# Optimization experiments

Hardware: AMD Instinct MI355X
Metric: run time of the kernel (lower is better)

## Reference

```python
import jax, jax.numpy as jnp
import numpy as np
import math

B, T, D = 4, 8192, 512
E, K, F = 8, 2, 2048
CAP_FACTOR = 1.25


def setup_inputs() -> dict:
    key = jax.random.key(0)
    ks = jax.random.split(key, 4)
    return {
        "x": jax.random.normal(ks[0], (B, T, D), jnp.float32),
        "gate_w": jax.random.normal(ks[1], (E, D), jnp.float32) * 0.01,  # std=0.01 init
        "w1": jax.random.normal(ks[2], (E, D, F), jnp.float32) * (1.0 / np.sqrt(D)),
        "b1": jnp.zeros((E, F), jnp.float32),
        "w2": jax.random.normal(ks[3], (E, F, D), jnp.float32) * (1.0 / np.sqrt(F)),
        "b2": jnp.zeros((E, D), jnp.float32),
    }


def reference(x, gate_w, w1, b1, w2, b2):
    Bx, Tx, Dx = x.shape
    N = Bx * Tx
    C = math.ceil(CAP_FACTOR * N / E)  # per-expert capacity
    xf = x.reshape(N, Dx)

    # --- Router (eval mode: no noise) ---
    probs = jax.nn.softmax(xf @ gate_w.T, axis=-1)            # (N, E)
    topk_vals, topk_idx = jax.lax.top_k(probs, K)             # (N, K)
    topk_vals = topk_vals / topk_vals.sum(-1, keepdims=True)

    # --- Capacity-based dispatch: token-major, k-minor assignment order,
    #     matching the original serial double loop exactly. ---
    flat_e = topk_idx.reshape(N * K)                          # (NK,)
    onehot = jax.nn.one_hot(flat_e, E, dtype=jnp.int32)       # (NK, E)
    # slot within expert = number of earlier assignments to same expert
    pos = jnp.cumsum(onehot, axis=0)[jnp.arange(N * K), flat_e] - 1
    keep = pos < C                                            # tokens over capacity are dropped
    pos_safe = jnp.where(keep, pos, C)                        # route drops to pad slot C
    token_ids = jnp.repeat(jnp.arange(N), K)

    # --- Gather tokens into (E, C, D) expert buffers (slot C is trash) ---
    buf = jnp.zeros((E, C + 1, Dx), x.dtype).at[flat_e, pos_safe].set(xf[token_ids])
    expert_in = buf[:, :C]                                    # (E, C, D)

    # --- Per-expert FFN (exact GELU, dropout=0 in eval) ---
    h = jax.nn.gelu(jnp.einsum('ecd,edf->ecf', expert_in, w1) + b1[:, None, :],
                    approximate=False)                        # (E, C, F)
    expert_out = jnp.einsum('ecf,efd->ecd', h, w2) + b2[:, None, :]  # (E, C, D)

    # --- Weighted combine back to tokens ---
    gathered = expert_out[flat_e, jnp.minimum(pos_safe, C - 1)]      # (NK, D)
    w = (topk_vals.reshape(N * K) * keep).astype(x.dtype)            # zero for dropped
    out = (gathered * w[:, None]).reshape(N, K, Dx).sum(axis=1)      # (N, D)
    return out.reshape(Bx, Tx, Dx)
```

## Files before the change

kernel.cpp:

```cpp
#include <hip/hip_runtime.h>
#include <math.h>

#define Bx 4
#define Tt 8192
#define Nn (Bx * Tt)
#define Dd 512
#define Ee 8
#define Kk 2
#define Ff 2048
#define Cc 5120
#define NK (Nn * Kk)

typedef unsigned short ushort_t;
typedef __attribute__((ext_vector_type(8))) short bf16x8;
typedef __attribute__((ext_vector_type(4))) float f32x4;

__device__ __forceinline__ float gelu_exact(float v) {
    return 0.5f * v * (1.0f + erff(v * 0.70710678118654752440f));
}

__device__ __forceinline__ ushort_t f2bf(float f) {
    union { float f; unsigned u; } v; v.f = f;
    unsigned r = v.u + 0x7fffu + ((v.u >> 16) & 1u);
    return (ushort_t)(r >> 16);
}

__device__ __forceinline__ void gload_lds16(const ushort_t* g, short* l) {
    __builtin_amdgcn_global_load_lds(
        (const __attribute__((address_space(1))) unsigned int*)g,
        (__attribute__((address_space(3))) unsigned int*)l, 16, 0, 0);
}

__global__ __launch_bounds__(256) void moe_gate_kernel(
    const float* __restrict__ x, const float* __restrict__ gate_w,
    int* __restrict__ flat_e, float* __restrict__ wArr) {
    __shared__ float gw[Ee * Dd];
    int tid = threadIdx.x;
    for (int i = tid; i < 1024; i += 256)
        ((float4*)gw)[i] = ((const float4*)gate_w)[i];
    __syncthreads();

    int wave = tid >> 6, lane = tid & 63;
    int token = blockIdx.x * 4 + wave;

    const float4* xr = (const float4*)(x + (size_t)token * Dd);
    float4 xa = xr[lane];
    float4 xb = xr[lane + 64];

    float acc[Ee];
#pragma unroll
    for (int e = 0; e < Ee; e++) {
        const float4* g = (const float4*)(gw + e * Dd);
        float4 ga = g[lane], gb = g[lane + 64];
        acc[e] = xa.x * ga.x + xa.y * ga.y + xa.z * ga.z + xa.w * ga.w +
                 xb.x * gb.x + xb.y * gb.y + xb.z * gb.z + xb.w * gb.w;
    }
#pragma unroll
    for (int off = 32; off >= 1; off >>= 1) {
#pragma unroll
        for (int e = 0; e < Ee; e++) acc[e] += __shfl_xor(acc[e], off, 64);
    }

    if (lane == 0) {
        float m = acc[0];
#pragma unroll
        for (int e = 1; e < Ee; e++) m = fmaxf(m, acc[e]);
        float p[Ee], s = 0.f;
#pragma unroll
        for (int e = 0; e < Ee; e++) { p[e] = expf(acc[e] - m); s += p[e]; }
        int i0 = 0;
#pragma unroll
        for (int e = 1; e < Ee; e++) if (p[e] > p[i0]) i0 = e;
        int i1 = (i0 == 0) ? 1 : 0;
#pragma unroll
        for (int e = 0; e < Ee; e++) if (e != i0 && p[e] > p[i1]) i1 = e;
        float v0 = p[i0] / s, v1 = p[i1] / s;
        float inv = 1.f / (v0 + v1);
        flat_e[token * 2 + 0] = i0;
        flat_e[token * 2 + 1] = i1;
        wArr[token * 2 + 0] = v0 * inv;
        wArr[token * 2 + 1] = v1 * inv;
    }
}

__global__ __launch_bounds__(256) void moe_hist_kernel(
    const int* __restrict__ flat_e, int* __restrict__ blockCounts) {
    __shared__ int cnt[Ee];
    int tid = threadIdx.x;
    if (tid < Ee) cnt[tid] = 0;
    __syncthreads();
    int e = flat_e[blockIdx.x * 256 + tid];
    atomicAdd(&cnt[e], 1);
    __syncthreads();
    if (tid < Ee) blockCounts[blockIdx.x * Ee + tid] = cnt[tid];
}

__global__ void moe_scan_kernel(const int* __restrict__ blockCounts,
                                int* __restrict__ blockOffsets,
                                int* __restrict__ counts) {
    int e = threadIdx.x;
    if (e >= Ee) return;
    int run = 0;
    for (int b = 0; b < 256; b++) {
        blockOffsets[b * Ee + e] = run;
        run += blockCounts[b * Ee + e];
    }
    counts[e] = min(run, Cc);
}

__global__ __launch_bounds__(256) void moe_scatter_kernel(
    const int* __restrict__ flat_e, const float* __restrict__ wArr,
    const int* __restrict__ blockOffsets,
    int* __restrict__ srcOf, float* __restrict__ wSlot) {
    __shared__ int waveCnt[4][Ee];
    int tid = threadIdx.x;
    int i = blockIdx.x * 256 + tid;
    int e = flat_e[i];
    int wv = tid >> 6, lane = tid & 63;
    unsigned long long ltmask = (1ull << lane) - 1ull;
    int myrank = 0;
#pragma unroll
    for (int ee = 0; ee < Ee; ee++) {
        unsigned long long m = __ballot(e == ee);
        if (e == ee) myrank = __popcll(m & ltmask);
        if (lane == 0) waveCnt[wv][ee] = __popcll(m);
    }
    __syncthreads();
    int base = blockOffsets[blockIdx.x * Ee + e];
    for (int w = 0; w < wv; w++) base += waveCnt[w][e];
    int pos = base + myrank;
    if (pos < Cc) {
        srcOf[e * Cc + pos] = i >> 1;
        wSlot[e * Cc + pos] = wArr[i];
    }
}

__global__ __launch_bounds__(256) void moe_transpose_kernel(
    const float* __restrict__ in, ushort_t* __restrict__ out, int R, int Cn) {
    __shared__ float t[32][33];
    int ez = blockIdx.z;
    const float* ine = in + (size_t)ez * R * Cn;
    ushort_t* oute = out + (size_t)ez * R * Cn;
    int tx = threadIdx.x & 31, ty = threadIdx.x >> 5;
    int r0 = blockIdx.y * 32, c0 = blockIdx.x * 32;
#pragma unroll
    for (int j = 0; j < 4; j++)
        t[ty + j * 8][tx] = ine[(size_t)(r0 + ty + j * 8) * Cn + c0 + tx];
    __syncthreads();
#pragma unroll
    for (int j = 0; j < 4; j++)
        oute[(size_t)(c0 + ty + j * 8) * R + r0 + tx] = f2bf(t[tx][ty + j * 8]);
}

__global__ __launch_bounds__(256) void moe_gather_kernel(
    const float* __restrict__ x, const int* __restrict__ srcOf,
    const int* __restrict__ counts, int chunk0, ushort_t* __restrict__ xg) {
    int tid = threadIdx.x, wave = tid >> 6, lane = tid & 63;
    int sl = blockIdx.x * 4 + wave;
    int le = sl / Cc, c = sl - le * Cc;
    int e = chunk0 + le;
    int cnt = counts[e];
    ushort_t* dst = xg + (size_t)sl * Dd + lane * 8;
    uint4 o;
    if (c < cnt) {
        int src = srcOf[e * Cc + c];
        const float4* xr = (const float4*)(x + (size_t)src * Dd + lane * 8);
        float4 v0 = xr[0], v1 = xr[1];
        o.x = (unsigned)f2bf(v0.x) | ((unsigned)f2bf(v0.y) << 16);
        o.y = (unsigned)f2bf(v0.z) | ((unsigned)f2bf(v0.w) << 16);
        o.z = (unsigned)f2bf(v1.x) | ((unsigned)f2bf(v1.y) << 16);
        o.w = (unsigned)f2bf(v1.z) | ((unsigned)f2bf(v1.w) << 16);
    } else {
        o = make_uint4(0, 0, 0, 0);
    }
    *(uint4*)dst = o;
}


__global__ __launch_bounds__(256) void moe_mfma_gemm1(
    const ushort_t* __restrict__ xg, const ushort_t* __restrict__ w1t,
    const float* __restrict__ b1, int chunk0, ushort_t* __restrict__ hbuf) {
    int le = blockIdx.z, e = chunk0 + le;
    const ushort_t* A = xg + (size_t)le * Cc * Dd;
    const ushort_t* Bt = w1t + (size_t)e * Ff * Dd;
    const float* bias = b1 + (size_t)e * Ff;
    ushort_t* h = hbuf + (size_t)le * Cc * Ff;

    __shared__ short Al[4 * 128 * 8];
    __shared__ short Bl[4 * 128 * 8];

    int tid = threadIdx.x;
    int lane = tid & 63, wave = tid >> 6;
    int wr = wave >> 1, wc = wave & 1;
    int m0 = blockIdx.y * 128;
    int n0 = blockIdx.x * 128;
    int kslot = lane >> 4, lr = lane & 15;
    int aoff = (kslot * 128 + wr * 64 + lr) * 8;
    int boff = (kslot * 128 + wc * 64 + lr) * 8;
    int wbase = (tid & 192) * 8;

    f32x4 acc[4][4] = {};

    for (int k0 = 0; k0 < Dd; k0 += 32) {
#pragma unroll
        for (int p = 0; p < 2; ++p) {
            int id = p * 256 + tid;
            int ks = id >> 7, row = id & 127;
            gload_lds16(A + (size_t)(m0 + row) * Dd + k0 + ks * 8,
                        &Al[p * 2048 + wbase]);
            gload_lds16(Bt + (size_t)(n0 + row) * Dd + k0 + ks * 8,
                        &Bl[p * 2048 + wbase]);
        }
        __syncthreads();
        bf16x8 a[4], b[4];
#pragma unroll
        for (int m = 0; m < 4; ++m) a[m] = *(const bf16x8*)&Al[aoff + m * 128];
#pragma unroll
        for (int n = 0; n < 4; ++n) b[n] = *(const bf16x8*)&Bl[boff + n * 128];
#pragma unroll
        for (int m = 0; m < 4; ++m)
#pragma unroll
            for (int n = 0; n < 4; ++n)
                acc[m][n] = __builtin_amdgcn_mfma_f32_16x16x32_bf16(
                    a[m], b[n], acc[m][n], 0, 0, 0);
        __syncthreads();
    }

    float bv[4];
#pragma unroll
    for (int n = 0; n < 4; ++n) bv[n] = bias[n0 + wc * 64 + n * 16 + lr];
#pragma unroll
    for (int m = 0; m < 4; ++m) {
#pragma unroll
        for (int r = 0; r < 4; ++r) {
            int row = m0 + wr * 64 + m * 16 + kslot * 4 + r;
            size_t base = (size_t)row * Ff + n0 + wc * 64 + lr;
#pragma unroll
            for (int n = 0; n < 4; ++n)
                h[base + n * 16] = f2bf(gelu_exact(acc[m][n][r] + bv[n]));
        }
    }
}

__global__ __launch_bounds__(256) void moe_mfma_gemm2(
    const ushort_t* __restrict__ hbuf, const ushort_t* __restrict__ w2t,
    const float* __restrict__ b2, const int* __restrict__ srcOf,
    const float* __restrict__ wSlot, const int* __restrict__ counts,
    int chunk0, float* __restrict__ out) {
    int le = blockIdx.z, e = chunk0 + le;
    const ushort_t* A = hbuf + (size_t)le * Cc * Ff;
    const ushort_t* Bt = w2t + (size_t)e * Dd * Ff;
    const float* bias = b2 + (size_t)e * Dd;
    const int* srcE = srcOf + (size_t)e * Cc;
    const float* wE = wSlot + (size_t)e * Cc;
    int count = counts[e];

    __shared__ short Al[4 * 128 * 8];
    __shared__ short Bl[4 * 128 * 8];

    int tid = threadIdx.x;
    int lane = tid & 63, wave = tid >> 6;
    int wr = wave >> 1, wc = wave & 1;
    int m0 = blockIdx.y * 128;
    int n0 = blockIdx.x * 128;
    int kslot = lane >> 4, lr = lane & 15;
    int aoff = (kslot * 128 + wr * 64 + lr) * 8;
    int boff = (kslot * 128 + wc * 64 + lr) * 8;
    int wbase = (tid & 192) * 8;

    f32x4 acc[4][4] = {};

    for (int k0 = 0; k0 < Ff; k0 += 32) {
#pragma unroll
        for (int p = 0; p < 2; ++p) {
            int id = p * 256 + tid;
            int ks = id >> 7, row = id & 127;
            gload_lds16(A + (size_t)(m0 + row) * Ff + k0 + ks * 8,
                        &Al[p * 2048 + wbase]);
            gload_lds16(Bt + (size_t)(n0 + row) * Ff + k0 + ks * 8,
                        &Bl[p * 2048 + wbase]);
        }
        __syncthreads();
        bf16x8 a[4], b[4];
#pragma unroll
        for (int m = 0; m < 4; ++m) a[m] = *(const bf16x8*)&Al[aoff + m * 128];
#pragma unroll
        for (int n = 0; n < 4; ++n) b[n] = *(const bf16x8*)&Bl[boff + n * 128];
#pragma unroll
        for (int m = 0; m < 4; ++m)
#pragma unroll
            for (int n = 0; n < 4; ++n)
                acc[m][n] = __builtin_amdgcn_mfma_f32_16x16x32_bf16(
                    a[m], b[n], acc[m][n], 0, 0, 0);
        __syncthreads();
    }

    float bv[4];
#pragma unroll
    for (int n = 0; n < 4; ++n) bv[n] = bias[n0 + wc * 64 + n * 16 + lr];
#pragma unroll
    for (int m = 0; m < 4; ++m) {
#pragma unroll
        for (int r = 0; r < 4; ++r) {
            int row = m0 + wr * 64 + m * 16 + kslot * 4 + r;
            if (row < count) {
                int token = srcE[row];
                float wgt = wE[row];
                float* op = out + (size_t)token * Dd + n0 + wc * 64 + lr;
#pragma unroll
                for (int n = 0; n < 4; ++n)
                    atomicAdd(&op[n * 16], wgt * (acc[m][n][r] + bv[n]));
            }
        }
    }
}

extern "C" void kernel_launch(void* const* d_in, const int* in_sizes, int n_in,
                              void* d_out, int out_size, void* d_ws, size_t ws_size,
                              hipStream_t stream) {
    const float* x      = (const float*)d_in[0];
    const float* gate_w = (const float*)d_in[1];
    const float* w1     = (const float*)d_in[2];
    const float* b1     = (const float*)d_in[3];
    const float* w2     = (const float*)d_in[4];
    const float* b2     = (const float*)d_in[5];
    float* out = (float*)d_out;

    char* p = (char*)d_ws;
    int*      flat_e       = (int*)p;       p += (size_t)NK * 4;
    float*    wArr         = (float*)p;     p += (size_t)NK * 4;
    int*      blockCounts  = (int*)p;       p += 256 * Ee * 4;
    int*      blockOffsets = (int*)p;       p += 256 * Ee * 4;
    int*      counts       = (int*)p;       p += 64 * 4;
    int*      srcOf        = (int*)p;       p += (size_t)Ee * Cc * 4;
    float*    wSlot        = (float*)p;     p += (size_t)Ee * Cc * 4;
    p = (char*)(((size_t)p + 255) & ~(size_t)255);
    ushort_t* w1t          = (ushort_t*)p;  p += (size_t)Ee * Dd * Ff * 2;
    ushort_t* w2t          = (ushort_t*)p;  p += (size_t)Ee * Ff * Dd * 2;
    size_t fixedEnd = (size_t)(p - (char*)d_ws);
    size_t avail = (ws_size > fixedEnd) ? ws_size - fixedEnd : 0;

    size_t perE = (size_t)Cc * Dd * 2 + (size_t)Cc * Ff * 2;
    int P = Ee;
    while (P > 1 && (size_t)P * perE > avail) P >>= 1;
    ushort_t* xg = (ushort_t*)((char*)d_ws + fixedEnd);
    ushort_t* hbuf = xg + (size_t)P * Cc * Dd;

    moe_gate_kernel<<<Nn / 4, 256, 0, stream>>>(x, gate_w, flat_e, wArr);
    moe_hist_kernel<<<NK / 256, 256, 0, stream>>>(flat_e, blockCounts);
    moe_scan_kernel<<<1, 64, 0, stream>>>(blockCounts, blockOffsets, counts);
    moe_scatter_kernel<<<NK / 256, 256, 0, stream>>>(flat_e, wArr, blockOffsets,
                                                     srcOf, wSlot);
    moe_transpose_kernel<<<dim3(Ff / 32, Dd / 32, Ee), 256, 0, stream>>>(
        w1, w1t, Dd, Ff);
    moe_transpose_kernel<<<dim3(Dd / 32, Ff / 32, Ee), 256, 0, stream>>>(
        w2, w2t, Ff, Dd);
    hipMemsetAsync(d_out, 0, (size_t)Nn * Dd * sizeof(float), stream);

    for (int c0 = 0; c0 < Ee; c0 += P) {
        moe_gather_kernel<<<P * Cc / 4, 256, 0, stream>>>(x, srcOf, counts, c0, xg);
        moe_mfma_gemm1<<<dim3(Ff / 128, Cc / 128, P), 256, 0, stream>>>(
            xg, w1t, b1, c0, hbuf);
        moe_mfma_gemm2<<<dim3(Dd / 128, Cc / 128, P), 256, 0, stream>>>(
            hbuf, w2t, b2, srcOf, wSlot, counts, c0, out);
    }
}
```

Baseline: 685.8 us.

## Double-buffer LDS staging in both GEMMs and split-K gemm2 across two blocks

```diff
diff --git a/kernel.cpp b/kernel.cpp
--- a/kernel.cpp
+++ b/kernel.cpp
@@ -177,6 +177,15 @@
 }
 
 
+#define GSTAGE(gA, gB, Al, Bl, buf, t, wbase)                                  \
+    do {                                                                       \
+        int _k = (t) * 32;                                                     \
+        gload_lds16((gA) + _k,      &(Al)[(buf) * 4096 + (wbase)]);            \
+        gload_lds16((gA) + _k + 16, &(Al)[(buf) * 4096 + 2048 + (wbase)]);     \
+        gload_lds16((gB) + _k,      &(Bl)[(buf) * 4096 + (wbase)]);            \
+        gload_lds16((gB) + _k + 16, &(Bl)[(buf) * 4096 + 2048 + (wbase)]);     \
+    } while (0)
+
 __global__ __launch_bounds__(256) void moe_mfma_gemm1(
     const ushort_t* __restrict__ xg, const ushort_t* __restrict__ w1t,
     const float* __restrict__ b1, int chunk0, ushort_t* __restrict__ hbuf) {
@@ -186,8 +195,8 @@
     const float* bias = b1 + (size_t)e * Ff;
     ushort_t* h = hbuf + (size_t)le * Cc * Ff;
 
-    __shared__ short Al[4 * 128 * 8];
-    __shared__ short Bl[4 * 128 * 8];
+    __shared__ short Al[2 * 4096];
+    __shared__ short Bl[2 * 4096];
 
     int tid = threadIdx.x;
     int lane = tid & 63, wave = tid >> 6;
@@ -198,32 +207,39 @@
     int aoff = (kslot * 128 + wr * 64 + lr) * 8;
     int boff = (kslot * 128 + wc * 64 + lr) * 8;
     int wbase = (tid & 192) * 8;
+    int row = tid & 127, ks0 = tid >> 7;
+
+    const ushort_t* gA = A + (size_t)(m0 + row) * Dd + ks0 * 8;
+    const ushort_t* gB = Bt + (size_t)(n0 + row) * Dd + ks0 * 8;
 
     f32x4 acc[4][4] = {};
-
-    for (int k0 = 0; k0 < Dd; k0 += 32) {
-#pragma unroll
-        for (int p = 0; p < 2; ++p) {
-            int id = p * 256 + tid;
-            int ks = id >> 7, row = id & 127;
-            gload_lds16(A + (size_t)(m0 + row) * Dd + k0 + ks * 8,
-                        &Al[p * 2048 + wbase]);
-            gload_lds16(Bt + (size_t)(n0 + row) * Dd + k0 + ks * 8,
-                        &Bl[p * 2048 + wbase]);
+    const int NT = Dd / 32;
+
+    GSTAGE(gA, gB, Al, Bl, 0, 0, wbase);
+    for (int t = 0; t < NT; ++t) {
+        int cur = t & 1;
+        if (t + 1 < NT) {
+            GSTAGE(gA, gB, Al, Bl, cur ^ 1, t + 1, wbase);
+            asm volatile("s_waitcnt vmcnt(4)" ::: "memory");
+        } else {
+            asm volatile("s_waitcnt vmcnt(0)" ::: "memory");
         }
-        __syncthreads();
+        __builtin_amdgcn_s_barrier();
+        asm volatile("" ::: "memory");
         bf16x8 a[4], b[4];
-#pragma unroll
-        for (int m = 0; m < 4; ++m) a[m] = *(const bf16x8*)&Al[aoff + m * 128];
-#pragma unroll
-        for (int n = 0; n < 4; ++n) b[n] = *(const bf16x8*)&Bl[boff + n * 128];
+        int ab = cur * 4096 + aoff, bb = cur * 4096 + boff;
+#pragma unroll
+        for (int m = 0; m < 4; ++m) a[m] = *(const bf16x8*)&Al[ab + m * 128];
+#pragma unroll
+        for (int n = 0; n < 4; ++n) b[n] = *(const bf16x8*)&Bl[bb + n * 128];
 #pragma unroll
         for (int m = 0; m < 4; ++m)
 #pragma unroll
             for (int n = 0; n < 4; ++n)
                 acc[m][n] = __builtin_amdgcn_mfma_f32_16x16x32_bf16(
                     a[m], b[n], acc[m][n], 0, 0, 0);
-        __syncthreads();
+        asm volatile("" ::: "memory");
+        __builtin_amdgcn_s_barrier();
     }
 
     float bv[4];
@@ -233,8 +249,8 @@
     for (int m = 0; m < 4; ++m) {
 #pragma unroll
         for (int r = 0; r < 4; ++r) {
-            int row = m0 + wr * 64 + m * 16 + kslot * 4 + r;
-            size_t base = (size_t)row * Ff + n0 + wc * 64 + lr;
+            int orow = m0 + wr * 64 + m * 16 + kslot * 4 + r;
+            size_t base = (size_t)orow * Ff + n0 + wc * 64 + lr;
 #pragma unroll
             for (int n = 0; n < 4; ++n)
                 h[base + n * 16] = f2bf(gelu_exact(acc[m][n][r] + bv[n]));
@@ -247,16 +263,19 @@
     const float* __restrict__ b2, const int* __restrict__ srcOf,
     const float* __restrict__ wSlot, const int* __restrict__ counts,
     int chunk0, float* __restrict__ out) {
-    int le = blockIdx.z, e = chunk0 + le;
-    const ushort_t* A = hbuf + (size_t)le * Cc * Ff;
-    const ushort_t* Bt = w2t + (size_t)e * Dd * Ff;
+    int z = blockIdx.z;
+    int le = z >> 1, ksp = z & 1;
+    int e = chunk0 + le;
+    const int KH = Ff / 2;
+    const ushort_t* A = hbuf + (size_t)le * Cc * Ff + (size_t)ksp * KH;
+    const ushort_t* Bt = w2t + (size_t)e * Dd * Ff + (size_t)ksp * KH;
     const float* bias = b2 + (size_t)e * Dd;
     const int* srcE = srcOf + (size_t)e * Cc;
     const float* wE = wSlot + (size_t)e * Cc;
     int count = counts[e];
 
-    __shared__ short Al[4 * 128 * 8];
-    __shared__ short Bl[4 * 128 * 8];
+    __shared__ short Al[2 * 4096];
+    __shared__ short Bl[2 * 4096];
 
     int tid = threadIdx.x;
     int lane = tid & 63, wave = tid >> 6;
@@ -267,45 +286,53 @@
     int aoff = (kslot * 128 + wr * 64 + lr) * 8;
     int boff = (kslot * 128 + wc * 64 + lr) * 8;
     int wbase = (tid & 192) * 8;
+    int row = tid & 127, ks0 = tid >> 7;
+
+    const ushort_t* gA = A + (size_t)(m0 + row) * Ff + ks0 * 8;
+    const ushort_t* gB = Bt + (size_t)(n0 + row) * Ff + ks0 * 8;
 
     f32x4 acc[4][4] = {};
-
-    for (int k0 = 0; k0 < Ff; k0 += 32) {
-#pragma unroll
-        for (int p = 0; p < 2; ++p) {
-            int id = p * 256 + tid;
-            int ks = id >> 7, row = id & 127;
-            gload_lds16(A + (size_t)(m0 + row) * Ff + k0 + ks * 8,
-                        &Al[p * 2048 + wbase]);
-            gload_lds16(Bt + (size_t)(n0 + row) * Ff + k0 + ks * 8,
-                        &Bl[p * 2048 + wbase]);
+    const int NT = KH / 32;
+
+    GSTAGE(gA, gB, Al, Bl, 0, 0, wbase);
+    for (int t = 0; t < NT; ++t) {
+        int cur = t & 1;
+        if (t + 1 < NT) {
+            GSTAGE(gA, gB, Al, Bl, cur ^ 1, t + 1, wbase);
+            asm volatile("s_waitcnt vmcnt(4)" ::: "memory");
+        } else {
+            asm volatile("s_waitcnt vmcnt(0)" ::: "memory");
         }
-        __syncthreads();
+        __builtin_amdgcn_s_barrier();
+        asm volatile("" ::: "memory");
         bf16x8 a[4], b[4];
-#pragma unroll
-        for (int m = 0; m < 4; ++m) a[m] = *(const bf16x8*)&Al[aoff + m * 128];
-#pragma unroll
-        for (int n = 0; n < 4; ++n) b[n] = *(const bf16x8*)&Bl[boff + n * 128];
+        int ab = cur * 4096 + aoff, bb = cur * 4096 + boff;
+#pragma unroll
+        for (int m = 0; m < 4; ++m) a[m] = *(const bf16x8*)&Al[ab + m * 128];
+#pragma unroll
+        for (int n = 0; n < 4; ++n) b[n] = *(const bf16x8*)&Bl[bb + n * 128];
 #pragma unroll
         for (int m = 0; m < 4; ++m)
 #pragma unroll
             for (int n = 0; n < 4; ++n)
                 acc[m][n] = __builtin_amdgcn_mfma_f32_16x16x32_bf16(
                     a[m], b[n], acc[m][n], 0, 0, 0);
-        __syncthreads();
+        asm volatile("" ::: "memory");
+        __builtin_amdgcn_s_barrier();
     }
 
     float bv[4];
 #pragma unroll
-    for (int n = 0; n < 4; ++n) bv[n] = bias[n0 + wc * 64 + n * 16 + lr];
+    for (int n = 0; n < 4; ++n)
+        bv[n] = (ksp == 0) ? bias[n0 + wc * 64 + n * 16 + lr] : 0.f;
 #pragma unroll
     for (int m = 0; m < 4; ++m) {
 #pragma unroll
         for (int r = 0; r < 4; ++r) {
-            int row = m0 + wr * 64 + m * 16 + kslot * 4 + r;
-            if (row < count) {
-                int token = srcE[row];
-                float wgt = wE[row];
+            int orow = m0 + wr * 64 + m * 16 + kslot * 4 + r;
+            if (orow < count) {
+                int token = srcE[orow];
+                float wgt = wE[orow];
                 float* op = out + (size_t)token * Dd + n0 + wc * 64 + lr;
 #pragma unroll
                 for (int n = 0; n < 4; ++n)
@@ -361,7 +388,7 @@
         moe_gather_kernel<<<P * Cc / 4, 256, 0, stream>>>(x, srcOf, counts, c0, xg);
         moe_mfma_gemm1<<<dim3(Ff / 128, Cc / 128, P), 256, 0, stream>>>(
             xg, w1t, b1, c0, hbuf);
-        moe_mfma_gemm2<<<dim3(Dd / 128, Cc / 128, P), 256, 0, stream>>>(
+        moe_mfma_gemm2<<<dim3(Dd / 128, Cc / 128, P * 2), 256, 0, stream>>>(
             hbuf, w2t, b2, srcOf, wSlot, counts, c0, out);
     }
 }
```

Result: slower. 708.3 us (+3.3%).
